# Kernel optimization log

Measured on AMD Instinct MI355X. Metric: run time of the kernel, lower is better.

The kernel has to match this reference:

```python
import jax, jax.numpy as jnp
import numpy as np

B, S, H = 2, 2048, 1024
E, I = 8, 4096
TOP_K = 2
W_SCALE = 0.02


def setup_inputs() -> dict:
    key = jax.random.key(0)
    k1, k2, k3, k4, k5 = jax.random.split(key, 5)
    return {
        "hidden_states": jax.random.normal(k1, (B, S, H), dtype=jnp.float32),
        "gate_w": jax.random.normal(k2, (H, E), dtype=jnp.float32) * W_SCALE,
        "w1s": jax.random.normal(k3, (E, H, I), dtype=jnp.float32) * W_SCALE,
        "w2s": jax.random.normal(k4, (E, I, H), dtype=jnp.float32) * W_SCALE,
        "w3s": jax.random.normal(k5, (E, H, I), dtype=jnp.float32) * W_SCALE,
    }


def reference(hidden_states, gate_w, w1s, w2s, w3s):
    b, s, h = hidden_states.shape
    x = hidden_states.reshape(-1, h)                      # [T, H]
    # Router: softmax in fp32, top-k, renormalize (matches torch F.softmax(dtype=float) + topk)
    logits = x @ gate_w                                   # [T, E]
    probs = jax.nn.softmax(logits.astype(jnp.float32), axis=-1)
    rw, sel = jax.lax.top_k(probs, TOP_K)                 # [T, K], [T, K]
    rw = rw / jnp.sum(rw, axis=-1, keepdims=True)
    # Per-token combine weight for each expert: [T, E]
    comb = jnp.sum(jax.nn.one_hot(sel, E, dtype=x.dtype) * rw[..., None].astype(x.dtype), axis=1)
    # Expert SwiGLU MLPs; loop over small fixed expert count (same math as grouped GEMM + scatter)
    out = jnp.zeros_like(x)
    for e in range(E):
        inter = jax.nn.silu(x @ w1s[e]) * (x @ w3s[e])    # [T, I]
        out = out + comb[:, e:e + 1] * (inter @ w2s[e])   # [T, H]
    return out.reshape(b, s, h)
```

## Files before the change

### kernel.cpp

```cpp
#include <hip/hip_runtime.h>

#define T_TOK 4096
#define H_DIM 1024
#define I_DIM 4096
#define NE 8
#define INTER_ROWS 9216

typedef _Float16 f16;
typedef _Float16 f16x8 __attribute__((ext_vector_type(8)));
typedef _Float16 f16x4 __attribute__((ext_vector_type(4)));
typedef float f32x4 __attribute__((ext_vector_type(4)));

#define GLOBAL_AS __attribute__((address_space(1)))
#define LDS_AS __attribute__((address_space(3)))

__device__ __forceinline__ void gload_lds16(const void* g, void* l) {
  __builtin_amdgcn_global_load_lds((GLOBAL_AS const unsigned int*)g,
                                   (LDS_AS unsigned int*)l, 16, 0, 0);
}

#define VM6() asm volatile("s_waitcnt vmcnt(6)" ::: "memory")
#define VM4() asm volatile("s_waitcnt vmcnt(4)" ::: "memory")
#define VM0() asm volatile("s_waitcnt vmcnt(0)" ::: "memory")
#define BAR() __builtin_amdgcn_s_barrier()
#define PRIO1() __builtin_amdgcn_s_setprio(1)
#define PRIO0() __builtin_amdgcn_s_setprio(0)

__global__ void cast_x_kernel(const float* __restrict__ x, f16* __restrict__ xh) {
  int i = blockIdx.x * 256 + threadIdx.x;
  float4 v = reinterpret_cast<const float4*>(x)[i];
  f16x4 o = {(f16)v.x, (f16)v.y, (f16)v.z, (f16)v.w};
  reinterpret_cast<f16x4*>(xh)[i] = o;
}

__global__ __launch_bounds__(256) void transpose_cast_kernel(
    const float* __restrict__ w1s, const float* __restrict__ w3s,
    const float* __restrict__ w2s, f16* __restrict__ w13t, f16* __restrict__ w2t) {
  __shared__ float tile[64][65];
  const int z = blockIdx.z;
  const int tr = threadIdx.x >> 4;
  const int tc = (threadIdx.x & 15) * 4;
  if (z < 16) {
    int e = z & 7;
    const float* in = (z < 8 ? w1s : w3s) + (size_t)e * H_DIM * I_DIM;
    f16* out = w13t + (size_t)e * (2 * H_DIM * I_DIM);
    const int roff = (z < 8) ? 0 : 32;
    const int c0 = blockIdx.x * 64, r0 = blockIdx.y * 64;
#pragma unroll
    for (int i = 0; i < 4; ++i) {
      int r = tr + i * 16;
      float4 v = *reinterpret_cast<const float4*>(&in[(size_t)(r0 + r) * I_DIM + c0 + tc]);
      tile[r][tc] = v.x; tile[r][tc + 1] = v.y; tile[r][tc + 2] = v.z; tile[r][tc + 3] = v.w;
    }
    __syncthreads();
#pragma unroll
    for (int i = 0; i < 4; ++i) {
      int oc = tr + i * 16;
      int cg = c0 + oc;
      int rowo = ((cg >> 5) << 6) + roff + (cg & 31);
      f16x4 h;
#pragma unroll
      for (int j = 0; j < 4; ++j) h[j] = (f16)tile[tc + j][oc];
      *reinterpret_cast<f16x4*>(&out[(size_t)rowo * H_DIM + r0 + tc]) = h;
    }
  } else {
    int e = z - 16;
    const float* in = w2s + (size_t)e * H_DIM * I_DIM;
    f16* out = w2t + (size_t)e * H_DIM * I_DIM;
    const int r0 = blockIdx.x * 64, c0 = blockIdx.y * 64;
#pragma unroll
    for (int i = 0; i < 4; ++i) {
      int r = tr + i * 16;
      float4 v = *reinterpret_cast<const float4*>(&in[(size_t)(r0 + r) * H_DIM + c0 + tc]);
      tile[r][tc] = v.x; tile[r][tc + 1] = v.y; tile[r][tc + 2] = v.z; tile[r][tc + 3] = v.w;
    }
    __syncthreads();
#pragma unroll
    for (int i = 0; i < 4; ++i) {
      int oc = tr + i * 16;
      f16x4 h;
#pragma unroll
      for (int j = 0; j < 4; ++j) h[j] = (f16)tile[tc + j][oc];
      *reinterpret_cast<f16x4*>(&out[(size_t)(c0 + oc) * I_DIM + r0 + tc]) = h;
    }
  }
}

__global__ void router_kernel(const float* __restrict__ x, const float* __restrict__ gw,
                              int* __restrict__ counts, int* __restrict__ lists,
                              float* __restrict__ wgts) {
  const int t = blockIdx.x;
  const int l = threadIdx.x;
  const float* xr = x + (size_t)t * H_DIM;
  float acc[NE];
#pragma unroll
  for (int e = 0; e < NE; ++e) acc[e] = 0.f;
  for (int k = l; k < H_DIM; k += 64) {
    float xv = xr[k];
#pragma unroll
    for (int e = 0; e < NE; ++e) acc[e] += xv * gw[k * NE + e];
  }
#pragma unroll
  for (int e = 0; e < NE; ++e) {
    float v = acc[e];
#pragma unroll
    for (int off = 32; off > 0; off >>= 1) v += __shfl_xor(v, off);
    acc[e] = v;
  }
  if (l == 0) {
    int i1 = 0;
#pragma unroll
    for (int e = 1; e < NE; ++e)
      if (acc[e] > acc[i1]) i1 = e;
    int i2 = (i1 == 0) ? 1 : 0;
#pragma unroll
    for (int e = 0; e < NE; ++e)
      if (e != i1 && acc[e] > acc[i2]) i2 = e;
    float wA = 1.f / (1.f + __expf(acc[i2] - acc[i1]));
    float wB = 1.f - wA;
    int p1 = atomicAdd(&counts[i1], 1);
    lists[i1 * T_TOK + p1] = t;
    wgts[i1 * T_TOK + p1] = wA;
    int p2 = atomicAdd(&counts[i2], 1);
    lists[i2 * T_TOK + p2] = t;
    wgts[i2 * T_TOK + p2] = wB;
  }
}

__global__ void prefix_kernel(const int* __restrict__ counts, int* __restrict__ bases) {
  if (threadIdx.x == 0) {
    int s = 0;
#pragma unroll
    for (int e = 0; e < NE; ++e) {
      bases[e] = s;
      s += (counts[e] + 127) & ~127;
    }
  }
}

__global__ __launch_bounds__(512, 2) void gemm_a_kernel(
    const f16* __restrict__ xh, const f16* __restrict__ w13t,
    const int* __restrict__ counts, const int* __restrict__ bases,
    const int* __restrict__ lists, f16* __restrict__ inter) {
  const int z = blockIdx.z;
  const int cnt = counts[z];
  const int r0 = blockIdx.y * 256;
  if (r0 >= cnt) return;
  const int base = bases[z];
  const int pad = (cnt + 127) & ~127;
  const int c0 = blockIdx.x * 256;
  const int tid = threadIdx.x;
  const int lane = tid & 63;
  const int wid = tid >> 6;
  const int wm = wid >> 2, wn = wid & 3;
  const int lrow = lane & 15, lk = lane >> 4;

  __shared__ __align__(16) f16 ring[3][16384];

  const int* lst = lists + z * T_TOK;
  const f16* w13 = w13t + (size_t)z * (2 * H_DIM * I_DIM);

  const f16 *asrc[2], *bsrc[2];
#pragma unroll
  for (int i = 0; i < 2; ++i) {
    int sf = i * 512 + tid;
    int row = sf >> 2;
    int sl = (sf & 3) ^ ((row >> 1) & 3);
    int tok = lst[r0 + row];
    asrc[i] = xh + (size_t)tok * H_DIM + sl * 8;
    bsrc[i] = w13 + (size_t)(c0 + row) * H_DIM + sl * 8;
  }

#define STG(S, K)                                                     \
  do {                                                                \
    _Pragma("unroll") for (int i_ = 0; i_ < 2; ++i_)                  \
      gload_lds16(asrc[i_] + (K), (S) + (i_ * 512 + wid * 64) * 8);   \
    _Pragma("unroll") for (int i_ = 0; i_ < 2; ++i_)                  \
      gload_lds16(bsrc[i_] + (K), (S) + 8192 + (i_ * 512 + wid * 64) * 8); \
  } while (0)

  const f32x4 z4 = {0.f, 0.f, 0.f, 0.f};
  f32x4 acc[8][4];
#pragma unroll
  for (int m = 0; m < 8; ++m)
#pragma unroll
    for (int n = 0; n < 4; ++n) acc[m][n] = z4;

  f16 *s0 = ring[0], *s1 = ring[1], *s2 = ring[2];
  const int NT = H_DIM / 32;
  STG(s0, 0);
  STG(s1, 32);
  VM4();
  BAR();

  for (int t = 0; t < NT; ++t) {
    if (t + 2 < NT) STG(s2, (t + 2) * 32);
    f16x8 af[8], bf[4];
#pragma unroll
    for (int m = 0; m < 8; ++m) {
      int row = wm * 128 + m * 16 + lrow;
      af[m] = *reinterpret_cast<const f16x8*>(&s0[(row * 4 + (lk ^ ((row >> 1) & 3))) * 8]);
    }
#pragma unroll
    for (int n = 0; n < 4; ++n) {
      int row = wn * 64 + n * 16 + lrow;
      bf[n] = *reinterpret_cast<const f16x8*>(&s0[8192 + (row * 4 + (lk ^ ((row >> 1) & 3))) * 8]);
    }
    PRIO1();
#pragma unroll
    for (int m = 0; m < 8; ++m)
#pragma unroll
      for (int n = 0; n < 4; ++n)
        acc[m][n] = __builtin_amdgcn_mfma_f32_16x16x32_f16(af[m], bf[n], acc[m][n], 0, 0, 0);
    PRIO0();
    if (t + 2 < NT) VM4(); else VM0();
    BAR();
    f16* tmp = s0; s0 = s1; s1 = s2; s2 = tmp;
  }
#undef STG

#pragma unroll
  for (int m = 0; m < 8; ++m)
#pragma unroll
    for (int r = 0; r < 4; ++r) {
      int rowl = wm * 128 + m * 16 + lk * 4 + r;
      if (r0 + rowl < pad) {
        size_t grow = base + r0 + rowl;
#pragma unroll
        for (int n = 0; n < 2; ++n) {
          int col = (c0 >> 1) + wn * 32 + n * 16 + lrow;
          float v1 = acc[m][n][r];
          float v3 = acc[m][n + 2][r];
          float sv = v1 / (1.f + __expf(-v1));
          inter[grow * I_DIM + col] = (f16)(sv * v3);
        }
      }
    }
}

__global__ __launch_bounds__(256, 2) void gemm_b_kernel(
    const f16* __restrict__ inter, const f16* __restrict__ w2t,
    const int* __restrict__ counts, const int* __restrict__ bases,
    const int* __restrict__ lists, const float* __restrict__ wgts,
    float* __restrict__ out) {
  const int z = blockIdx.z;
  const int cnt = counts[z];
  const int rb = blockIdx.y >> 1, kb = blockIdx.y & 1;
  const int r0 = rb * 256;
  if (r0 >= cnt) return;
  const int base = bases[z];
  const int c0 = blockIdx.x * 128;
  const int tid = threadIdx.x;
  const int lane = tid & 63;
  const int wid = tid >> 6;
  const int wm = wid >> 1, wn = wid & 1;
  const int lrow = lane & 15, lk = lane >> 4;

  __shared__ __align__(16) f16 ring[3][12288];

  const int* lst = lists + z * T_TOK;
  const float* wgt = wgts + z * T_TOK;
  const f16* w2 = w2t + (size_t)z * I_DIM * H_DIM;
  const int k0 = kb * 2048;

  const f16* asrc[4];
#pragma unroll
  for (int i = 0; i < 4; ++i) {
    int sf = i * 256 + tid;
    int row = sf >> 2;
    int sl = (sf & 3) ^ ((row >> 1) & 3);
    int gr = base + r0 + row;
    if (gr > INTER_ROWS - 1) gr = INTER_ROWS - 1;
    asrc[i] = inter + (size_t)gr * I_DIM + k0 + sl * 8;
  }
  const f16* bsrc[2];
#pragma unroll
  for (int i = 0; i < 2; ++i) {
    int sf = i * 256 + tid;
    int row = sf >> 2;
    int sl = (sf & 3) ^ ((row >> 1) & 3);
    bsrc[i] = w2 + (size_t)(c0 + row) * I_DIM + k0 + sl * 8;
  }

#define STG(S, K)                                                     \
  do {                                                                \
    _Pragma("unroll") for (int i_ = 0; i_ < 4; ++i_)                  \
      gload_lds16(asrc[i_] + (K), (S) + (i_ * 256 + wid * 64) * 8);   \
    _Pragma("unroll") for (int i_ = 0; i_ < 2; ++i_)                  \
      gload_lds16(bsrc[i_] + (K), (S) + 8192 + (i_ * 256 + wid * 64) * 8); \
  } while (0)

  const f32x4 z4 = {0.f, 0.f, 0.f, 0.f};
  f32x4 acc[8][4];
#pragma unroll
  for (int m = 0; m < 8; ++m)
#pragma unroll
    for (int n = 0; n < 4; ++n) acc[m][n] = z4;

  f16 *s0 = ring[0], *s1 = ring[1], *s2 = ring[2];
  const int NT = 2048 / 32;
  STG(s0, 0);
  STG(s1, 32);
  VM6();
  BAR();

  for (int t = 0; t < NT; ++t) {
    if (t + 2 < NT) STG(s2, (t + 2) * 32);
    f16x8 af[8], bf[4];
#pragma unroll
    for (int m = 0; m < 8; ++m) {
      int row = wm * 128 + m * 16 + lrow;
      af[m] = *reinterpret_cast<const f16x8*>(&s0[(row * 4 + (lk ^ ((row >> 1) & 3))) * 8]);
    }
#pragma unroll
    for (int n = 0; n < 4; ++n) {
      int row = wn * 64 + n * 16 + lrow;
      bf[n] = *reinterpret_cast<const f16x8*>(&s0[8192 + (row * 4 + (lk ^ ((row >> 1) & 3))) * 8]);
    }
    PRIO1();
#pragma unroll
    for (int m = 0; m < 8; ++m)
#pragma unroll
      for (int n = 0; n < 4; ++n)
        acc[m][n] = __builtin_amdgcn_mfma_f32_16x16x32_f16(af[m], bf[n], acc[m][n], 0, 0, 0);
    PRIO0();
    if (t + 2 < NT) VM6(); else VM0();
    BAR();
    f16* tmp = s0; s0 = s1; s1 = s2; s2 = tmp;
  }
#undef STG

#pragma unroll
  for (int m = 0; m < 8; ++m)
#pragma unroll
    for (int r = 0; r < 4; ++r) {
      int ri = r0 + wm * 128 + m * 16 + lk * 4 + r;
      if (ri < cnt) {
        int tok = lst[ri];
        float wg = wgt[ri];
        float* orow = out + (size_t)tok * H_DIM + c0 + wn * 64 + lrow;
#pragma unroll
        for (int n = 0; n < 4; ++n) atomicAdd(&orow[n * 16], wg * acc[m][n][r]);
      }
    }
}

extern "C" void kernel_launch(void* const* d_in, const int* in_sizes, int n_in,
                              void* d_out, int out_size, void* d_ws, size_t ws_size,
                              hipStream_t stream) {
  const float* x = (const float*)d_in[0];
  const float* gw = (const float*)d_in[1];
  const float* w1s = (const float*)d_in[2];
  const float* w2s = (const float*)d_in[3];
  const float* w3s = (const float*)d_in[4];
  float* out = (float*)d_out;

  char* ws = (char*)d_ws;
  f16* xh = (f16*)ws;
  f16* inter = (f16*)(ws + ((size_t)8 << 20));
  f16* w13t = (f16*)(ws + ((size_t)80 << 20));
  f16* w2t = (f16*)(ws + ((size_t)208 << 20));
  char* meta = ws + ((size_t)272 << 20);
  int* counts = (int*)meta;
  int* bases = (int*)(meta + 512);
  int* lists = (int*)(meta + 1024);
  float* wgts = (float*)(meta + 1024 + (size_t)NE * T_TOK * 4);

  hipMemsetAsync(out, 0, (size_t)out_size * sizeof(float), stream);
  hipMemsetAsync(meta, 0, 1024 + (size_t)NE * T_TOK * 8, stream);

  cast_x_kernel<<<dim3((T_TOK * H_DIM) / (4 * 256)), dim3(256), 0, stream>>>(x, xh);
  router_kernel<<<dim3(T_TOK), dim3(64), 0, stream>>>(x, gw, counts, lists, wgts);
  prefix_kernel<<<dim3(1), dim3(64), 0, stream>>>(counts, bases);
  transpose_cast_kernel<<<dim3(64, 16, 24), dim3(256), 0, stream>>>(
      w1s, w3s, w2s, w13t, w2t);
  gemm_a_kernel<<<dim3((2 * I_DIM) / 256, T_TOK / 256, NE), dim3(512), 0, stream>>>(
      xh, w13t, counts, bases, lists, inter);
  gemm_b_kernel<<<dim3(H_DIM / 128, 2 * (T_TOK / 256), NE), dim3(256), 0, stream>>>(
      inter, w2t, counts, bases, lists, wgts, out);
}
```

Measured before the change: 566.1 us.

## Restructure expert GEMMs into double-buffered K=64 pipeline with 256x256 tiles

Both grouped GEMM kernels move from a 3-stage ring with K=32 steps to a 2-buffer, K=64 scheme that splits each step into four phases. Global-to-LDS loads for the next tile are issued between MFMA sub-batches, separated by barriers. The LDS layout switches to a 64-wide row with XOR-8 swizzle. gemm_b grows to 512 threads with 256x256 tiles, and both kernels drop to one block per CU. The goal is better overlap of loads with MFMA and more reuse per tile. The cost is more barriers, a full vmcnt(0) wait every step, and lower occupancy.

```diff
diff --git a/kernel.cpp b/kernel.cpp
--- a/kernel.cpp
+++ b/kernel.cpp
@@ -19,10 +19,13 @@
                                    (LDS_AS unsigned int*)l, 16, 0, 0);
 }
 
-#define VM6() asm volatile("s_waitcnt vmcnt(6)" ::: "memory")
-#define VM4() asm volatile("s_waitcnt vmcnt(4)" ::: "memory")
 #define VM0() asm volatile("s_waitcnt vmcnt(0)" ::: "memory")
-#define BAR() __builtin_amdgcn_s_barrier()
+#define BARF()                          \
+  do {                                  \
+    asm volatile("" ::: "memory");      \
+    __builtin_amdgcn_s_barrier();       \
+    asm volatile("" ::: "memory");      \
+  } while (0)
 #define PRIO1() __builtin_amdgcn_s_setprio(1)
 #define PRIO0() __builtin_amdgcn_s_setprio(0)
 
@@ -138,7 +141,7 @@
   }
 }
 
-__global__ __launch_bounds__(512, 2) void gemm_a_kernel(
+__global__ __launch_bounds__(512, 1) void gemm_a_kernel(
     const f16* __restrict__ xh, const f16* __restrict__ w13t,
     const int* __restrict__ counts, const int* __restrict__ bases,
     const int* __restrict__ lists, f16* __restrict__ inter) {
@@ -146,38 +149,65 @@
   const int cnt = counts[z];
   const int r0 = blockIdx.y * 256;
   if (r0 >= cnt) return;
-  const int base = bases[z];
-  const int pad = (cnt + 127) & ~127;
+  const int base = bases[z], pad = (cnt + 127) & ~127;
   const int c0 = blockIdx.x * 256;
-  const int tid = threadIdx.x;
-  const int lane = tid & 63;
-  const int wid = tid >> 6;
-  const int wm = wid >> 2, wn = wid & 3;
-  const int lrow = lane & 15, lk = lane >> 4;
-
-  __shared__ __align__(16) f16 ring[3][16384];
+  const int tid = threadIdx.x, lane = tid & 63, wid = tid >> 6;
+  const int wm = wid >> 2, wn = wid & 3, lrow = lane & 15, lk = lane >> 4;
+
+  __shared__ __align__(16) f16 lds[2][32768];
 
   const int* lst = lists + z * T_TOK;
   const f16* w13 = w13t + (size_t)z * (2 * H_DIM * I_DIM);
 
-  const f16 *asrc[2], *bsrc[2];
-#pragma unroll
-  for (int i = 0; i < 2; ++i) {
-    int sf = i * 512 + tid;
-    int row = sf >> 2;
-    int sl = (sf & 3) ^ ((row >> 1) & 3);
-    int tok = lst[r0 + row];
-    asrc[i] = xh + (size_t)tok * H_DIM + sl * 8;
-    bsrc[i] = w13 + (size_t)(c0 + row) * H_DIM + sl * 8;
-  }
-
-#define STG(S, K)                                                     \
-  do {                                                                \
-    _Pragma("unroll") for (int i_ = 0; i_ < 2; ++i_)                  \
-      gload_lds16(asrc[i_] + (K), (S) + (i_ * 512 + wid * 64) * 8);   \
-    _Pragma("unroll") for (int i_ = 0; i_ < 2; ++i_)                  \
-      gload_lds16(bsrc[i_] + (K), (S) + 8192 + (i_ * 512 + wid * 64) * 8); \
+  const f16* sp[4][2];
+  f16* dp[4][2];
+#pragma unroll
+  for (int j = 0; j < 2; ++j) {
+    int cg = (wid * 2 + j) * 64 + lane;
+    int rih = cg >> 3;
+    int loct = (cg & 7) ^ (rih & 7);
+    int t0 = lst[r0 + rih], t1 = lst[r0 + 128 + rih];
+    sp[0][j] = xh + (size_t)t0 * H_DIM + loct * 8;
+    sp[2][j] = xh + (size_t)t1 * H_DIM + loct * 8;
+    sp[1][j] = w13 + (size_t)(c0 + rih) * H_DIM + loct * 8;
+    sp[3][j] = w13 + (size_t)(c0 + 128 + rih) * H_DIM + loct * 8;
+    dp[0][j] = &lds[0][cg * 8];
+    dp[2][j] = &lds[0][8192 + cg * 8];
+    dp[1][j] = &lds[0][16384 + cg * 8];
+    dp[3][j] = &lds[0][24576 + cg * 8];
+  }
+
+#define STG(u, S, K)                                        \
+  do {                                                      \
+    gload_lds16(sp[u][0] + (K), dp[u][0] + (S) * 32768);    \
+    gload_lds16(sp[u][1] + (K), dp[u][1] + (S) * 32768);    \
   } while (0)
+
+#define LDA(kh)                                                                        \
+  {                                                                                    \
+    _Pragma("unroll") for (int m_ = 0; m_ < 8; ++m_) {                                 \
+      int row = wm * 128 + m_ * 16 + lrow;                                             \
+      af[m_] = *reinterpret_cast<const f16x8*>(                                        \
+          &SA[row * 64 + (((kh) * 4 + lk) ^ (row & 7)) * 8]);                          \
+    }                                                                                  \
+  }
+#define LDB(kh, np)                                                                    \
+  {                                                                                    \
+    _Pragma("unroll") for (int n_ = 0; n_ < 2; ++n_) {                                 \
+      int row = wn * 64 + ((np) * 2 + n_) * 16 + lrow;                                 \
+      bf[n_] = *reinterpret_cast<const f16x8*>(                                        \
+          &SB[row * 64 + (((kh) * 4 + lk) ^ (row & 7)) * 8]);                          \
+    }                                                                                  \
+  }
+#define MF(np)                                                                         \
+  {                                                                                    \
+    PRIO1();                                                                           \
+    _Pragma("unroll") for (int m_ = 0; m_ < 8; ++m_)                                   \
+        _Pragma("unroll") for (int n_ = 0; n_ < 2; ++n_)                               \
+            acc[m_][(np) * 2 + n_] = __builtin_amdgcn_mfma_f32_16x16x32_f16(           \
+                af[m_], bf[n_], acc[m_][(np) * 2 + n_], 0, 0, 0);                      \
+    PRIO0();                                                                           \
+  }
 
   const f32x4 z4 = {0.f, 0.f, 0.f, 0.f};
   f32x4 acc[8][4];
@@ -186,38 +216,31 @@
 #pragma unroll
     for (int n = 0; n < 4; ++n) acc[m][n] = z4;
 
-  f16 *s0 = ring[0], *s1 = ring[1], *s2 = ring[2];
-  const int NT = H_DIM / 32;
-  STG(s0, 0);
-  STG(s1, 32);
-  VM4();
-  BAR();
+  const int NT = H_DIM / 64;
+  STG(0, 0, 0); STG(1, 0, 0); STG(2, 0, 0); STG(3, 0, 0);
 
   for (int t = 0; t < NT; ++t) {
-    if (t + 2 < NT) STG(s2, (t + 2) * 32);
-    f16x8 af[8], bf[4];
-#pragma unroll
-    for (int m = 0; m < 8; ++m) {
-      int row = wm * 128 + m * 16 + lrow;
-      af[m] = *reinterpret_cast<const f16x8*>(&s0[(row * 4 + (lk ^ ((row >> 1) & 3))) * 8]);
-    }
-#pragma unroll
-    for (int n = 0; n < 4; ++n) {
-      int row = wn * 64 + n * 16 + lrow;
-      bf[n] = *reinterpret_cast<const f16x8*>(&s0[8192 + (row * 4 + (lk ^ ((row >> 1) & 3))) * 8]);
-    }
-    PRIO1();
-#pragma unroll
-    for (int m = 0; m < 8; ++m)
-#pragma unroll
-      for (int n = 0; n < 4; ++n)
-        acc[m][n] = __builtin_amdgcn_mfma_f32_16x16x32_f16(af[m], bf[n], acc[m][n], 0, 0, 0);
-    PRIO0();
-    if (t + 2 < NT) VM4(); else VM0();
-    BAR();
-    f16* tmp = s0; s0 = s1; s1 = s2; s2 = tmp;
+    const f16* SA = lds[t & 1];
+    const f16* SB = SA + 16384;
+    const int S = (t + 1) & 1;
+    const int ks = (t + 1 < NT ? t + 1 : NT - 1) * 64;
+    f16x8 af[8], bf[2];
+    VM0();
+    BARF();
+    STG(0, S, ks); STG(1, S, ks);
+    LDA(0); LDB(0, 0); MF(0);
+    BARF();
+    STG(2, S, ks); STG(3, S, ks);
+    LDB(0, 1); MF(1);
+    BARF();
+    LDA(1); LDB(1, 0); MF(0);
+    BARF();
+    LDB(1, 1); MF(1);
   }
 #undef STG
+#undef LDA
+#undef LDB
+#undef MF
 
 #pragma unroll
   for (int m = 0; m < 8; ++m)
@@ -238,7 +261,7 @@
     }
 }
 
-__global__ __launch_bounds__(256, 2) void gemm_b_kernel(
+__global__ __launch_bounds__(512, 1) void gemm_b_kernel(
     const f16* __restrict__ inter, const f16* __restrict__ w2t,
     const int* __restrict__ counts, const int* __restrict__ bases,
     const int* __restrict__ lists, const float* __restrict__ wgts,
@@ -249,46 +272,65 @@
   const int r0 = rb * 256;
   if (r0 >= cnt) return;
   const int base = bases[z];
-  const int c0 = blockIdx.x * 128;
-  const int tid = threadIdx.x;
-  const int lane = tid & 63;
-  const int wid = tid >> 6;
-  const int wm = wid >> 1, wn = wid & 1;
-  const int lrow = lane & 15, lk = lane >> 4;
-
-  __shared__ __align__(16) f16 ring[3][12288];
+  const int c0 = blockIdx.x * 256;
+  const int tid = threadIdx.x, lane = tid & 63, wid = tid >> 6;
+  const int wm = wid >> 2, wn = wid & 3, lrow = lane & 15, lk = lane >> 4;
+
+  __shared__ __align__(16) f16 lds[2][32768];
 
   const int* lst = lists + z * T_TOK;
   const float* wgt = wgts + z * T_TOK;
   const f16* w2 = w2t + (size_t)z * I_DIM * H_DIM;
-  const int k0 = kb * 2048;
-
-  const f16* asrc[4];
-#pragma unroll
-  for (int i = 0; i < 4; ++i) {
-    int sf = i * 256 + tid;
-    int row = sf >> 2;
-    int sl = (sf & 3) ^ ((row >> 1) & 3);
-    int gr = base + r0 + row;
-    if (gr > INTER_ROWS - 1) gr = INTER_ROWS - 1;
-    asrc[i] = inter + (size_t)gr * I_DIM + k0 + sl * 8;
-  }
-  const f16* bsrc[2];
-#pragma unroll
-  for (int i = 0; i < 2; ++i) {
-    int sf = i * 256 + tid;
-    int row = sf >> 2;
-    int sl = (sf & 3) ^ ((row >> 1) & 3);
-    bsrc[i] = w2 + (size_t)(c0 + row) * I_DIM + k0 + sl * 8;
-  }
-
-#define STG(S, K)                                                     \
-  do {                                                                \
-    _Pragma("unroll") for (int i_ = 0; i_ < 4; ++i_)                  \
-      gload_lds16(asrc[i_] + (K), (S) + (i_ * 256 + wid * 64) * 8);   \
-    _Pragma("unroll") for (int i_ = 0; i_ < 2; ++i_)                  \
-      gload_lds16(bsrc[i_] + (K), (S) + 8192 + (i_ * 256 + wid * 64) * 8); \
+  const int K0 = kb * 2048;
+
+  const f16* sp[4][2];
+  f16* dp[4][2];
+#pragma unroll
+  for (int j = 0; j < 2; ++j) {
+    int cg = (wid * 2 + j) * 64 + lane;
+    int rih = cg >> 3;
+    int loct = (cg & 7) ^ (rih & 7);
+    sp[0][j] = inter + (size_t)(base + r0 + rih) * I_DIM + K0 + loct * 8;
+    sp[2][j] = inter + (size_t)(base + r0 + 128 + rih) * I_DIM + K0 + loct * 8;
+    sp[1][j] = w2 + (size_t)(c0 + rih) * I_DIM + K0 + loct * 8;
+    sp[3][j] = w2 + (size_t)(c0 + 128 + rih) * I_DIM + K0 + loct * 8;
+    dp[0][j] = &lds[0][cg * 8];
+    dp[2][j] = &lds[0][8192 + cg * 8];
+    dp[1][j] = &lds[0][16384 + cg * 8];
+    dp[3][j] = &lds[0][24576 + cg * 8];
+  }
+
+#define STG(u, S, K)                                        \
+  do {                                                      \
+    gload_lds16(sp[u][0] + (K), dp[u][0] + (S) * 32768);    \
+    gload_lds16(sp[u][1] + (K), dp[u][1] + (S) * 32768);    \
   } while (0)
+
+#define LDA(kh)                                                                        \
+  {                                                                                    \
+    _Pragma("unroll") for (int m_ = 0; m_ < 8; ++m_) {                                 \
+      int row = wm * 128 + m_ * 16 + lrow;                                             \
+      af[m_] = *reinterpret_cast<const f16x8*>(                                        \
+          &SA[row * 64 + (((kh) * 4 + lk) ^ (row & 7)) * 8]);                          \
+    }                                                                                  \
+  }
+#define LDB(kh, np)                                                                    \
+  {                                                                                    \
+    _Pragma("unroll") for (int n_ = 0; n_ < 2; ++n_) {                                 \
+      int row = wn * 64 + ((np) * 2 + n_) * 16 + lrow;                                 \
+      bf[n_] = *reinterpret_cast<const f16x8*>(                                        \
+          &SB[row * 64 + (((kh) * 4 + lk) ^ (row & 7)) * 8]);                          \
+    }                                                                                  \
+  }
+#define MF(np)                                                                         \
+  {                                                                                    \
+    PRIO1();                                                                           \
+    _Pragma("unroll") for (int m_ = 0; m_ < 8; ++m_)                                   \
+        _Pragma("unroll") for (int n_ = 0; n_ < 2; ++n_)                               \
+            acc[m_][(np) * 2 + n_] = __builtin_amdgcn_mfma_f32_16x16x32_f16(           \
+                af[m_], bf[n_], acc[m_][(np) * 2 + n_], 0, 0, 0);                      \
+    PRIO0();                                                                           \
+  }
 
   const f32x4 z4 = {0.f, 0.f, 0.f, 0.f};
   f32x4 acc[8][4];
@@ -297,38 +339,31 @@
 #pragma unroll
     for (int n = 0; n < 4; ++n) acc[m][n] = z4;
 
-  f16 *s0 = ring[0], *s1 = ring[1], *s2 = ring[2];
-  const int NT = 2048 / 32;
-  STG(s0, 0);
-  STG(s1, 32);
-  VM6();
-  BAR();
+  const int NT = 2048 / 64;
+  STG(0, 0, 0); STG(1, 0, 0); STG(2, 0, 0); STG(3, 0, 0);
 
   for (int t = 0; t < NT; ++t) {
-    if (t + 2 < NT) STG(s2, (t + 2) * 32);
-    f16x8 af[8], bf[4];
-#pragma unroll
-    for (int m = 0; m < 8; ++m) {
-      int row = wm * 128 + m * 16 + lrow;
-      af[m] = *reinterpret_cast<const f16x8*>(&s0[(row * 4 + (lk ^ ((row >> 1) & 3))) * 8]);
-    }
-#pragma unroll
-    for (int n = 0; n < 4; ++n) {
-      int row = wn * 64 + n * 16 + lrow;
-      bf[n] = *reinterpret_cast<const f16x8*>(&s0[8192 + (row * 4 + (lk ^ ((row >> 1) & 3))) * 8]);
-    }
-    PRIO1();
-#pragma unroll
-    for (int m = 0; m < 8; ++m)
-#pragma unroll
-      for (int n = 0; n < 4; ++n)
-        acc[m][n] = __builtin_amdgcn_mfma_f32_16x16x32_f16(af[m], bf[n], acc[m][n], 0, 0, 0);
-    PRIO0();
-    if (t + 2 < NT) VM6(); else VM0();
-    BAR();
-    f16* tmp = s0; s0 = s1; s1 = s2; s2 = tmp;
+    const f16* SA = lds[t & 1];
+    const f16* SB = SA + 16384;
+    const int S = (t + 1) & 1;
+    const int ks = (t + 1 < NT ? t + 1 : NT - 1) * 64;
+    f16x8 af[8], bf[2];
+    VM0();
+    BARF();
+    STG(0, S, ks); STG(1, S, ks);
+    LDA(0); LDB(0, 0); MF(0);
+    BARF();
+    STG(2, S, ks); STG(3, S, ks);
+    LDB(0, 1); MF(1);
+    BARF();
+    LDA(1); LDB(1, 0); MF(0);
+    BARF();
+    LDB(1, 1); MF(1);
   }
 #undef STG
+#undef LDA
+#undef LDB
+#undef MF
 
 #pragma unroll
   for (int m = 0; m < 8; ++m)
@@ -376,6 +411,6 @@
       w1s, w3s, w2s, w13t, w2t);
   gemm_a_kernel<<<dim3((2 * I_DIM) / 256, T_TOK / 256, NE), dim3(512), 0, stream>>>(
       xh, w13t, counts, bases, lists, inter);
-  gemm_b_kernel<<<dim3(H_DIM / 128, 2 * (T_TOK / 256), NE), dim3(256), 0, stream>>>(
+  gemm_b_kernel<<<dim3(H_DIM / 256, 2 * (T_TOK / 256), NE), dim3(512), 0, stream>>>(
       inter, w2t, counts, bases, lists, wgts, out);
 }
```

After: 549.1 us. 3.0% less time.
